# Performance work log

Hardware: AMD Instinct MI355X
Metric: run time of the kernel (lower is better)

Reference implementation:

```python
import jax, jax.numpy as jnp
import numpy as np

D_MODEL = 768
NUM_HEADS = 12
DEPTH = D_MODEL // NUM_HEADS


def setup_inputs() -> dict:
    key = jax.random.key(0)
    ks = jax.random.split(key, 11)
    B, S, D = 2, 2048, D_MODEL
    scale = 1.0 / np.sqrt(D)
    inp = {
        "v": jax.random.normal(ks[0], (B, S, D), jnp.float32),
        "k": jax.random.normal(ks[1], (B, S, D), jnp.float32),
        "q": jax.random.normal(ks[2], (B, S, D), jnp.float32),
        "wq": jax.random.normal(ks[3], (D, D), jnp.float32) * scale,
        "bq": jnp.zeros((D,), jnp.float32),
        "wk": jax.random.normal(ks[4], (D, D), jnp.float32) * scale,
        "bk": jnp.zeros((D,), jnp.float32),
        "wv": jax.random.normal(ks[5], (D, D), jnp.float32) * scale,
        "bv": jnp.zeros((D,), jnp.float32),
        "wo": jax.random.normal(ks[6], (D, D), jnp.float32) * scale,
        "bo": jnp.zeros((D,), jnp.float32),
    }
    return inp


def _split_heads(x):
    # (B, S, D) -> (B, H, S, depth)
    B, S, _ = x.shape
    return x.reshape(B, S, NUM_HEADS, DEPTH).transpose(0, 2, 1, 3)


def reference(v, k, q, wq, bq, wk, bk, wv, bv, wo, bo):
    B, S, D = q.shape
    qh = _split_heads(q @ wq + bq)  # (B,H,S,dh)
    kh = _split_heads(k @ wk + bk)
    vh = _split_heads(v @ wv + bv)
    logits = jnp.einsum("bhqd,bhkd->bhqk", qh, kh) / jnp.sqrt(
        jnp.asarray(DEPTH, qh.dtype)
    )
    attn = jax.nn.softmax(logits, axis=-1)  # (B,H,S,S)
    ctx = jnp.einsum("bhqk,bhkd->bhqd", attn, vh)
    ctx = ctx.transpose(0, 2, 1, 3).reshape(B, S, D)
    return ctx @ wo + bo
```

## Files before the change

kernel.cpp:

```cpp
#include <hip/hip_runtime.h>
#include <hip/hip_bf16.h>
#include <math.h>

typedef __bf16 bf16;
typedef __attribute__((ext_vector_type(8))) __bf16 bf16x8;
typedef __attribute__((ext_vector_type(4))) __bf16 bf16x4v;
typedef __attribute__((ext_vector_type(4))) float f32x4;

#define MFMA16(a, b, c) __builtin_amdgcn_mfma_f32_16x16x32_bf16(a, b, c, 0, 0, 0)

__device__ __forceinline__ void gld16(const bf16* g, bf16* l) {
  __builtin_amdgcn_global_load_lds((const __attribute__((address_space(1))) void*)g,
                                   (__attribute__((address_space(3))) void*)l, 16, 0, 0);
}

__global__ __launch_bounds__(256) void prep(const float* __restrict__ q,
                                            const float* __restrict__ k,
                                            const float* __restrict__ v,
                                            bf16* __restrict__ qb, bf16* __restrict__ kb,
                                            bf16* __restrict__ vb,
                                            const float* __restrict__ w0,
                                            const float* __restrict__ w1,
                                            const float* __restrict__ w2,
                                            const float* __restrict__ w3,
                                            bf16* __restrict__ t0, bf16* __restrict__ t1,
                                            bf16* __restrict__ t2, bf16* __restrict__ t3) {
  const int lin = blockIdx.x;
  if (lin < 4608) {
    const int which = lin / 1536, idx = lin % 1536;
    const float* a = which == 0 ? q : (which == 1 ? k : v);
    bf16* o = which == 0 ? qb : (which == 1 ? kb : vb);
    const size_t i = ((size_t)idx * 256 + threadIdx.x) * 8;
    const float4 f0 = *(const float4*)(a + i);
    const float4 f1 = *(const float4*)(a + i + 4);
    bf16x8 r = {(bf16)f0.x, (bf16)f0.y, (bf16)f0.z, (bf16)f0.w,
                (bf16)f1.x, (bf16)f1.y, (bf16)f1.z, (bf16)f1.w};
    *(bf16x8*)(o + i) = r;
  } else {
    const int w = lin - 4608;
    const int z = w / 576, rem = w % 576;
    const int by = rem / 24, bx = rem % 24;
    const float* W = z == 0 ? w0 : (z == 1 ? w1 : (z == 2 ? w2 : w3));
    bf16* T = z == 0 ? t0 : (z == 1 ? t1 : (z == 2 ? t2 : t3));
    __shared__ float t[32][33];
    const int tx = threadIdx.x & 31, ty = threadIdx.x >> 5;
    const int c0 = bx * 32, r0 = by * 32;
#pragma unroll
    for (int i = 0; i < 4; ++i) {
      const int r = ty + 8 * i;
      t[r][tx] = W[(size_t)(r0 + r) * 768 + c0 + tx];
    }
    __syncthreads();
#pragma unroll
    for (int i = 0; i < 4; ++i) {
      const int r = ty + 8 * i;
      T[(size_t)(c0 + r) * 768 + r0 + tx] = (bf16)t[tx][r];
    }
  }
}

__device__ __forceinline__ void gemm_core(const bf16* __restrict__ A, const bf16* __restrict__ BT,
                                          int row0, int col0, bf16* As, bf16* Bs,
                                          f32x4 acc[4][4]) {
  const int tid = threadIdx.x;
  const int lane = tid & 63, wave = tid >> 6;
  const int m15 = lane & 15, kg = lane >> 4;
  const int wm = wave >> 1, wn = wave & 1;
  const int pr16 = lane & 15;
  const int pk8 = (lane >> 4) * 8;
#pragma unroll
  for (int i = 0; i < 4; ++i)
#pragma unroll
    for (int j = 0; j < 4; ++j) acc[i][j] = f32x4{0.f, 0.f, 0.f, 0.f};

  for (int k0 = 0; k0 < 768; k0 += 32) {
#pragma unroll
    for (int j = 0; j < 2; ++j) {
      const int i = wave * 2 + j;
      gld16(A + (size_t)(row0 + 16 * i + pr16) * 768 + k0 + pk8, As + i * 512);
      gld16(BT + (size_t)(col0 + 16 * i + pr16) * 768 + k0 + pk8, Bs + i * 512);
    }
    __syncthreads();
    bf16x8 af[4], bfr[4];
#pragma unroll
    for (int t = 0; t < 4; ++t)
      af[t] = *(const bf16x8*)(As + (4 * wm + t) * 512 + kg * 128 + m15 * 8);
#pragma unroll
    for (int t = 0; t < 4; ++t)
      bfr[t] = *(const bf16x8*)(Bs + (4 * wn + t) * 512 + kg * 128 + m15 * 8);
#pragma unroll
    for (int mt = 0; mt < 4; ++mt)
#pragma unroll
      for (int nt = 0; nt < 4; ++nt) acc[mt][nt] = MFMA16(af[mt], bfr[nt], acc[mt][nt]);
    __syncthreads();
  }
}

__global__ __launch_bounds__(256, 3) void gemm_qkv(
    const bf16* __restrict__ qb, const bf16* __restrict__ kb, const bf16* __restrict__ vb,
    const bf16* __restrict__ wqT, const bf16* __restrict__ wkT, const bf16* __restrict__ wvT,
    const float* __restrict__ bq, const float* __restrict__ bk, const float* __restrict__ bv,
    bf16* __restrict__ Qh, bf16* __restrict__ Kh, bf16* __restrict__ Vt) {
  __shared__ bf16 As[128 * 32], Bs[128 * 32];
  const bf16 *A, *BT;
  const float* bias;
  bf16* out;
  int mode;
  if (blockIdx.z == 0) { A = qb; BT = wqT; bias = bq; out = Qh; mode = 0; }
  else if (blockIdx.z == 1) { A = kb; BT = wkT; bias = bk; out = Kh; mode = 0; }
  else { A = vb; BT = wvT; bias = bv; out = Vt; mode = 1; }
  const int row0 = blockIdx.y * 128, col0 = blockIdx.x * 128;
  f32x4 acc[4][4];
  gemm_core(A, BT, row0, col0, As, Bs, acc);

  const int lane = threadIdx.x & 63, wave = threadIdx.x >> 6;
  const int m15 = lane & 15, kg = lane >> 4;
  const int wm = wave >> 1, wn = wave & 1;
#pragma unroll
  for (int mt = 0; mt < 4; ++mt) {
#pragma unroll
    for (int nt = 0; nt < 4; ++nt) {
      const int col = col0 + 64 * wn + 16 * nt + m15;
      const float bb = bias[col];
      const int h = col >> 6, d = col & 63;
      const int rowb = row0 + 64 * wm + 16 * mt + kg * 4;
      const int b = rowb >> 11, s0 = rowb & 2047;
      if (mode == 0) {
#pragma unroll
        for (int r = 0; r < 4; ++r)
          out[((size_t)(b * 12 + h) * 2048 + s0 + r) * 64 + d] = (bf16)(acc[mt][nt][r] + bb);
      } else {
        bf16x4v pk;
#pragma unroll
        for (int r = 0; r < 4; ++r) pk[r] = (bf16)(acc[mt][nt][r] + bb);
        *(bf16x4v*)&out[((size_t)(b * 12 + h) * 64 + d) * 2048 + s0] = pk;
      }
    }
  }
}

__global__ __launch_bounds__(256, 3) void gemm_out(const bf16* __restrict__ A,
                                                   const bf16* __restrict__ BT,
                                                   const float* __restrict__ bias,
                                                   float* __restrict__ out) {
  __shared__ bf16 As[64 * 32], Bs[64 * 32];
  const int tid = threadIdx.x;
  const int lane = tid & 63, wave = tid >> 6;
  const int m15 = lane & 15, kg = lane >> 4;
  const int wm = wave >> 1, wn = wave & 1;
  const int row0 = blockIdx.y * 64, col0 = blockIdx.x * 64;
  const int pr16 = lane & 15, pk8 = (lane >> 4) * 8;

  f32x4 acc[2][2];
#pragma unroll
  for (int i = 0; i < 2; ++i)
#pragma unroll
    for (int j = 0; j < 2; ++j) acc[i][j] = f32x4{0.f, 0.f, 0.f, 0.f};

  for (int k0 = 0; k0 < 768; k0 += 32) {
    gld16(A + (size_t)(row0 + 16 * wave + pr16) * 768 + k0 + pk8, As + wave * 512);
    gld16(BT + (size_t)(col0 + 16 * wave + pr16) * 768 + k0 + pk8, Bs + wave * 512);
    __syncthreads();
    bf16x8 af[2], bfr[2];
#pragma unroll
    for (int t = 0; t < 2; ++t)
      af[t] = *(const bf16x8*)(As + (2 * wm + t) * 512 + kg * 128 + m15 * 8);
#pragma unroll
    for (int t = 0; t < 2; ++t)
      bfr[t] = *(const bf16x8*)(Bs + (2 * wn + t) * 512 + kg * 128 + m15 * 8);
#pragma unroll
    for (int mt = 0; mt < 2; ++mt)
#pragma unroll
      for (int nt = 0; nt < 2; ++nt) acc[mt][nt] = MFMA16(af[mt], bfr[nt], acc[mt][nt]);
    __syncthreads();
  }
#pragma unroll
  for (int mt = 0; mt < 2; ++mt) {
#pragma unroll
    for (int nt = 0; nt < 2; ++nt) {
      const int col = col0 + 32 * wn + 16 * nt + m15;
      const float bb = bias[col];
#pragma unroll
      for (int r = 0; r < 4; ++r) {
        const int row = row0 + 32 * wm + 16 * mt + kg * 4 + r;
        out[(size_t)row * 768 + col] = acc[mt][nt][r] + bb;
      }
    }
  }
}

__global__ __launch_bounds__(256, 3) void attn_kernel(const bf16* __restrict__ Q,
                                                      const bf16* __restrict__ K,
                                                      const bf16* __restrict__ VT,
                                                      bf16* __restrict__ ctx) {
  __shared__ __align__(16) bf16 S[21504];

  const int tid = threadIdx.x;
  const int lane = tid & 63, wave = tid >> 6;
  const int m15 = lane & 15, kg = lane >> 4;
  const int lin = blockIdx.x;
  const int bh = lin % 24, qblk = lin / 24;
  const size_t hb = (size_t)bh * 2048 * 64;
  const bf16* Qp = Q + hb;
  const bf16* Kp = K + hb;
  const bf16* Vp = VT + hb;
  const int pipe = wave >> 1;
  const int qrow0 = qblk * 64 + (wave & 1) * 32;
  bf16* Pw = S + 16384 + wave * 1280;

  const int kpr = lane & 7, kpc = (lane >> 3) * 8;
  const int vpr = lane & 15, vpc = (lane >> 4) * 8;

  bf16x8 qf[2][2];
#pragma unroll
  for (int t = 0; t < 2; ++t)
#pragma unroll
    for (int ks = 0; ks < 2; ++ks) {
      bf16x8 tv = *(const bf16x8*)&Qp[(size_t)(qrow0 + 16 * t + m15) * 64 + 32 * ks + kg * 8];
#pragma unroll
      for (int j = 0; j < 8; ++j) tv[j] = (bf16)((float)tv[j] * 0.125f);
      qf[t][ks] = tv;
    }

  f32x4 o[2][4];
  float lp[2][4];
#pragma unroll
  for (int t = 0; t < 2; ++t) {
#pragma unroll
    for (int nt = 0; nt < 4; ++nt) o[t][nt] = f32x4{0.f, 0.f, 0.f, 0.f};
#pragma unroll
    for (int r = 0; r < 4; ++r) lp[t][r] = 0.f;
  }

#pragma unroll
  for (int j = 0; j < 4; ++j) {
    const int idx = wave * 4 + j;
    const int sp = idx >> 3, r8 = idx & 7;
    const int kc = sp * 1024;
    if (r8 < 4)
      gld16(Kp + (size_t)(kc + 8 * r8 + kpr) * 64 + kpc, S + sp * 2 * 2048 + r8 * 512);
    else {
      const int i = r8 - 4;
      gld16(Vp + (size_t)(16 * i + vpr) * 2048 + kc + vpc, S + 8192 + sp * 2 * 2048 + i * 512);
    }
  }

  for (int c = 0; c < 32; ++c) {
    const int buf = c & 1;
    __syncthreads();
    if (c < 31) {
      const int nb = buf ^ 1;
#pragma unroll
      for (int j = 0; j < 4; ++j) {
        const int idx = wave * 4 + j;
        const int sp = idx >> 3, r8 = idx & 7;
        const int kc = sp * 1024 + (c + 1) * 32;
        if (r8 < 4)
          gld16(Kp + (size_t)(kc + 8 * r8 + kpr) * 64 + kpc,
                S + (sp * 2 + nb) * 2048 + r8 * 512);
        else {
          const int i = r8 - 4;
          gld16(Vp + (size_t)(16 * i + vpr) * 2048 + kc + vpc,
                S + 8192 + (sp * 2 + nb) * 2048 + i * 512);
        }
      }
    }
    const bf16* KsB = S + (pipe * 2 + buf) * 2048;
    const bf16* VsB = S + 8192 + (pipe * 2 + buf) * 2048;

    f32x4 s[2][2];
#pragma unroll
    for (int t = 0; t < 2; ++t)
#pragma unroll
      for (int nt = 0; nt < 2; ++nt) s[t][nt] = f32x4{0.f, 0.f, 0.f, 0.f};
#pragma unroll
    for (int ks = 0; ks < 2; ++ks) {
#pragma unroll
      for (int nt = 0; nt < 2; ++nt) {
        const int key = 16 * nt + m15;
        const bf16x8 kf =
            *(const bf16x8*)&KsB[(key >> 3) * 512 + (4 * ks + kg) * 64 + (key & 7) * 8];
        s[0][nt] = MFMA16(qf[0][ks], kf, s[0][nt]);
        s[1][nt] = MFMA16(qf[1][ks], kf, s[1][nt]);
      }
    }
#pragma unroll
    for (int t = 0; t < 2; ++t)
#pragma unroll
      for (int r = 0; r < 4; ++r)
#pragma unroll
        for (int nt = 0; nt < 2; ++nt) {
          const float pe = __expf(s[t][nt][r]);
          lp[t][r] += pe;
          Pw[t * 640 + (kg * 4 + r) * 40 + 16 * nt + m15] = (bf16)pe;
        }
    asm volatile("s_waitcnt lgkmcnt(0)" ::: "memory");
    const bf16x8 pf0 = *(const bf16x8*)&Pw[0 * 640 + m15 * 40 + kg * 8];
    const bf16x8 pf1 = *(const bf16x8*)&Pw[1 * 640 + m15 * 40 + kg * 8];
#pragma unroll
    for (int nt = 0; nt < 4; ++nt) {
      const int d = 16 * nt + m15;
      const bf16x8 vf =
          *(const bf16x8*)&VsB[(d >> 4) * 512 + kg * 128 + (d & 15) * 8];
      o[0][nt] = MFMA16(pf0, vf, o[0][nt]);
      o[1][nt] = MFMA16(pf1, vf, o[1][nt]);
    }
  }

  __syncthreads();
  float* sc = (float*)S;
  if (wave >= 2) {
    const int rg = (wave - 2) * 2560;
#pragma unroll
    for (int t = 0; t < 2; ++t)
#pragma unroll
      for (int nt = 0; nt < 4; ++nt)
        *(f32x4*)&sc[rg + (t * 4 + nt) * 256 + lane * 4] = o[t][nt];
    f32x4 l0 = {lp[0][0], lp[0][1], lp[0][2], lp[0][3]};
    f32x4 l1 = {lp[1][0], lp[1][1], lp[1][2], lp[1][3]};
    *(f32x4*)&sc[rg + 2048 + lane * 8] = l0;
    *(f32x4*)&sc[rg + 2048 + lane * 8 + 4] = l1;
  }
  __syncthreads();
  if (wave < 2) {
    const int rg = wave * 2560;
#pragma unroll
    for (int t = 0; t < 2; ++t)
#pragma unroll
      for (int nt = 0; nt < 4; ++nt) {
        const f32x4 po = *(const f32x4*)&sc[rg + (t * 4 + nt) * 256 + lane * 4];
#pragma unroll
        for (int j = 0; j < 4; ++j) o[t][nt][j] += po[j];
      }
    const f32x4 pl0 = *(const f32x4*)&sc[rg + 2048 + lane * 8];
    const f32x4 pl1 = *(const f32x4*)&sc[rg + 2048 + lane * 8 + 4];
#pragma unroll
    for (int r = 0; r < 4; ++r) { lp[0][r] += pl0[r]; lp[1][r] += pl1[r]; }
#pragma unroll
    for (int t = 0; t < 2; ++t)
#pragma unroll
      for (int r = 0; r < 4; ++r) {
#pragma unroll
        for (int st = 1; st < 16; st <<= 1) lp[t][r] += __shfl_xor(lp[t][r], st);
      }
    const int b = bh / 12, h = bh % 12;
#pragma unroll
    for (int t = 0; t < 2; ++t)
#pragma unroll
      for (int nt = 0; nt < 4; ++nt)
#pragma unroll
        for (int r = 0; r < 4; ++r) {
          const int sr = qrow0 + 16 * t + kg * 4 + r;
          ctx[((size_t)(b * 2048) + sr) * 768 + h * 64 + 16 * nt + m15] =
              (bf16)(o[t][nt][r] / lp[t][r]);
        }
  }
}

extern "C" void kernel_launch(void* const* d_in, const int* in_sizes, int n_in,
                              void* d_out, int out_size, void* d_ws, size_t ws_size,
                              hipStream_t stream) {
  const float* v = (const float*)d_in[0];
  const float* k = (const float*)d_in[1];
  const float* q = (const float*)d_in[2];
  const float* wq = (const float*)d_in[3];
  const float* bq = (const float*)d_in[4];
  const float* wk = (const float*)d_in[5];
  const float* bk = (const float*)d_in[6];
  const float* wv = (const float*)d_in[7];
  const float* bv = (const float*)d_in[8];
  const float* wo = (const float*)d_in[9];
  const float* bo = (const float*)d_in[10];

  char* ws = (char*)d_ws;
  const size_t SEG = (size_t)4096 * 768 * sizeof(bf16);
  const size_t WSEG = (size_t)768 * 768 * sizeof(bf16);
  bf16* Qh = (bf16*)(ws + 0 * SEG);
  bf16* Kh = (bf16*)(ws + 1 * SEG);
  bf16* Vt = (bf16*)(ws + 2 * SEG);
  bf16* qb = (bf16*)(ws + 3 * SEG);
  bf16* kb = (bf16*)(ws + 4 * SEG);
  bf16* vb = (bf16*)(ws + 5 * SEG);
  bf16* ctx = qb;
  bf16* wqT = (bf16*)(ws + 6 * SEG);
  bf16* wkT = (bf16*)(ws + 6 * SEG + WSEG);
  bf16* wvT = (bf16*)(ws + 6 * SEG + 2 * WSEG);
  bf16* woT = (bf16*)(ws + 6 * SEG + 3 * WSEG);

  prep<<<dim3(6912), 256, 0, stream>>>(q, k, v, qb, kb, vb, wq, wk, wv, wo,
                                       wqT, wkT, wvT, woT);
  gemm_qkv<<<dim3(6, 32, 3), 256, 0, stream>>>(qb, kb, vb, wqT, wkT, wvT, bq, bk, bv,
                                               Qh, Kh, Vt);
  attn_kernel<<<dim3(768), 256, 0, stream>>>(Qh, Kh, Vt, ctx);
  gemm_out<<<dim3(12, 64), 256, 0, stream>>>(ctx, woT, bo, (float*)d_out);
}
```

Baseline: 214.2 us.

## Load GEMM fragments directly from global, retile to 96 columns, use exp2 in attention

The QKV and output projection GEMMs drop LDS staging and barriers and read MFMA fragments straight from global memory, with 96-wide column tiles and new grid sizes. The attention kernel folds log2(e) into the Q scaling and uses exp2 instead of exp. Its accumulator arrays are also flattened into separate per-tile variables. The aim is to remove LDS round trips and sync overhead and to cheapen the exponentials, at the cost of redundant global/L2 traffic from losing cross-wave reuse.

```diff
diff --git a/kernel.cpp b/kernel.cpp
--- a/kernel.cpp
+++ b/kernel.cpp
@@ -59,73 +59,62 @@
   }
 }
 
-__device__ __forceinline__ void gemm_core(const bf16* __restrict__ A, const bf16* __restrict__ BT,
-                                          int row0, int col0, bf16* As, bf16* Bs,
-                                          f32x4 acc[4][4]) {
-  const int tid = threadIdx.x;
-  const int lane = tid & 63, wave = tid >> 6;
-  const int m15 = lane & 15, kg = lane >> 4;
-  const int wm = wave >> 1, wn = wave & 1;
-  const int pr16 = lane & 15;
-  const int pk8 = (lane >> 4) * 8;
-#pragma unroll
-  for (int i = 0; i < 4; ++i)
-#pragma unroll
-    for (int j = 0; j < 4; ++j) acc[i][j] = f32x4{0.f, 0.f, 0.f, 0.f};
-
-  for (int k0 = 0; k0 < 768; k0 += 32) {
-#pragma unroll
-    for (int j = 0; j < 2; ++j) {
-      const int i = wave * 2 + j;
-      gld16(A + (size_t)(row0 + 16 * i + pr16) * 768 + k0 + pk8, As + i * 512);
-      gld16(BT + (size_t)(col0 + 16 * i + pr16) * 768 + k0 + pk8, Bs + i * 512);
-    }
-    __syncthreads();
-    bf16x8 af[4], bfr[4];
-#pragma unroll
-    for (int t = 0; t < 4; ++t)
-      af[t] = *(const bf16x8*)(As + (4 * wm + t) * 512 + kg * 128 + m15 * 8);
-#pragma unroll
-    for (int t = 0; t < 4; ++t)
-      bfr[t] = *(const bf16x8*)(Bs + (4 * wn + t) * 512 + kg * 128 + m15 * 8);
-#pragma unroll
-    for (int mt = 0; mt < 4; ++mt)
-#pragma unroll
-      for (int nt = 0; nt < 4; ++nt) acc[mt][nt] = MFMA16(af[mt], bfr[nt], acc[mt][nt]);
-    __syncthreads();
-  }
-}
-
 __global__ __launch_bounds__(256, 3) void gemm_qkv(
     const bf16* __restrict__ qb, const bf16* __restrict__ kb, const bf16* __restrict__ vb,
     const bf16* __restrict__ wqT, const bf16* __restrict__ wkT, const bf16* __restrict__ wvT,
     const float* __restrict__ bq, const float* __restrict__ bk, const float* __restrict__ bv,
     bf16* __restrict__ Qh, bf16* __restrict__ Kh, bf16* __restrict__ Vt) {
-  __shared__ bf16 As[128 * 32], Bs[128 * 32];
   const bf16 *A, *BT;
   const float* bias;
-  bf16* out;
   int mode;
-  if (blockIdx.z == 0) { A = qb; BT = wqT; bias = bq; out = Qh; mode = 0; }
-  else if (blockIdx.z == 1) { A = kb; BT = wkT; bias = bk; out = Kh; mode = 0; }
-  else { A = vb; BT = wvT; bias = bv; out = Vt; mode = 1; }
-  const int row0 = blockIdx.y * 128, col0 = blockIdx.x * 128;
-  f32x4 acc[4][4];
-  gemm_core(A, BT, row0, col0, As, Bs, acc);
-
-  const int lane = threadIdx.x & 63, wave = threadIdx.x >> 6;
+  if (blockIdx.z == 0) { A = qb; BT = wqT; bias = bq; mode = 0; }
+  else if (blockIdx.z == 1) { A = kb; BT = wkT; bias = bk; mode = 0; }
+  else { A = vb; BT = wvT; bias = bv; mode = 1; }
+  const int row0 = blockIdx.y * 128, col0 = blockIdx.x * 96;
+
+  const int tid = threadIdx.x;
+  const int lane = tid & 63, wave = tid >> 6;
   const int m15 = lane & 15, kg = lane >> 4;
   const int wm = wave >> 1, wn = wave & 1;
+
+  const bf16* Ab[4];
+  const bf16* Bb[3];
+#pragma unroll
+  for (int t = 0; t < 4; ++t)
+    Ab[t] = A + (size_t)(row0 + 64 * wm + 16 * t + m15) * 768 + kg * 8;
+#pragma unroll
+  for (int t = 0; t < 3; ++t)
+    Bb[t] = BT + (size_t)(col0 + 48 * wn + 16 * t + m15) * 768 + kg * 8;
+
+  f32x4 acc[4][3];
+#pragma unroll
+  for (int i = 0; i < 4; ++i)
+#pragma unroll
+    for (int j = 0; j < 3; ++j) acc[i][j] = f32x4{0.f, 0.f, 0.f, 0.f};
+
+  for (int k0 = 0; k0 < 768; k0 += 32) {
+    bf16x8 af[4], bfr[3];
+#pragma unroll
+    for (int t = 0; t < 4; ++t) af[t] = *(const bf16x8*)(Ab[t] + k0);
+#pragma unroll
+    for (int t = 0; t < 3; ++t) bfr[t] = *(const bf16x8*)(Bb[t] + k0);
+#pragma unroll
+    for (int mt = 0; mt < 4; ++mt)
+#pragma unroll
+      for (int nt = 0; nt < 3; ++nt) acc[mt][nt] = MFMA16(af[mt], bfr[nt], acc[mt][nt]);
+  }
+
 #pragma unroll
   for (int mt = 0; mt < 4; ++mt) {
 #pragma unroll
-    for (int nt = 0; nt < 4; ++nt) {
-      const int col = col0 + 64 * wn + 16 * nt + m15;
+    for (int nt = 0; nt < 3; ++nt) {
+      const int col = col0 + 48 * wn + 16 * nt + m15;
       const float bb = bias[col];
       const int h = col >> 6, d = col & 63;
       const int rowb = row0 + 64 * wm + 16 * mt + kg * 4;
       const int b = rowb >> 11, s0 = rowb & 2047;
       if (mode == 0) {
+        bf16* out = (blockIdx.z == 0) ? Qh : Kh;
 #pragma unroll
         for (int r = 0; r < 4; ++r)
           out[((size_t)(b * 12 + h) * 2048 + s0 + r) * 64 + d] = (bf16)(acc[mt][nt][r] + bb);
@@ -133,52 +122,53 @@
         bf16x4v pk;
 #pragma unroll
         for (int r = 0; r < 4; ++r) pk[r] = (bf16)(acc[mt][nt][r] + bb);
-        *(bf16x4v*)&out[((size_t)(b * 12 + h) * 64 + d) * 2048 + s0] = pk;
-      }
-    }
-  }
-}
-
-__global__ __launch_bounds__(256, 3) void gemm_out(const bf16* __restrict__ A,
+        *(bf16x4v*)&Vt[((size_t)(b * 12 + h) * 64 + d) * 2048 + s0] = pk;
+      }
+    }
+  }
+}
+
+__global__ __launch_bounds__(256, 4) void gemm_out(const bf16* __restrict__ A,
                                                    const bf16* __restrict__ BT,
                                                    const float* __restrict__ bias,
                                                    float* __restrict__ out) {
-  __shared__ bf16 As[64 * 32], Bs[64 * 32];
   const int tid = threadIdx.x;
   const int lane = tid & 63, wave = tid >> 6;
   const int m15 = lane & 15, kg = lane >> 4;
   const int wm = wave >> 1, wn = wave & 1;
-  const int row0 = blockIdx.y * 64, col0 = blockIdx.x * 64;
-  const int pr16 = lane & 15, pk8 = (lane >> 4) * 8;
-
-  f32x4 acc[2][2];
+  const int row0 = blockIdx.y * 64, col0 = blockIdx.x * 96;
+
+  const bf16* Ab[2];
+  const bf16* Bb[3];
+#pragma unroll
+  for (int t = 0; t < 2; ++t)
+    Ab[t] = A + (size_t)(row0 + 32 * wm + 16 * t + m15) * 768 + kg * 8;
+#pragma unroll
+  for (int t = 0; t < 3; ++t)
+    Bb[t] = BT + (size_t)(col0 + 48 * wn + 16 * t + m15) * 768 + kg * 8;
+
+  f32x4 acc[2][3];
 #pragma unroll
   for (int i = 0; i < 2; ++i)
 #pragma unroll
-    for (int j = 0; j < 2; ++j) acc[i][j] = f32x4{0.f, 0.f, 0.f, 0.f};
+    for (int j = 0; j < 3; ++j) acc[i][j] = f32x4{0.f, 0.f, 0.f, 0.f};
 
   for (int k0 = 0; k0 < 768; k0 += 32) {
-    gld16(A + (size_t)(row0 + 16 * wave + pr16) * 768 + k0 + pk8, As + wave * 512);
-    gld16(BT + (size_t)(col0 + 16 * wave + pr16) * 768 + k0 + pk8, Bs + wave * 512);
-    __syncthreads();
-    bf16x8 af[2], bfr[2];
-#pragma unroll
-    for (int t = 0; t < 2; ++t)
-      af[t] = *(const bf16x8*)(As + (2 * wm + t) * 512 + kg * 128 + m15 * 8);
-#pragma unroll
-    for (int t = 0; t < 2; ++t)
-      bfr[t] = *(const bf16x8*)(Bs + (2 * wn + t) * 512 + kg * 128 + m15 * 8);
+    bf16x8 af[2], bfr[3];
+#pragma unroll
+    for (int t = 0; t < 2; ++t) af[t] = *(const bf16x8*)(Ab[t] + k0);
+#pragma unroll
+    for (int t = 0; t < 3; ++t) bfr[t] = *(const bf16x8*)(Bb[t] + k0);
 #pragma unroll
     for (int mt = 0; mt < 2; ++mt)
 #pragma unroll
-      for (int nt = 0; nt < 2; ++nt) acc[mt][nt] = MFMA16(af[mt], bfr[nt], acc[mt][nt]);
-    __syncthreads();
+      for (int nt = 0; nt < 3; ++nt) acc[mt][nt] = MFMA16(af[mt], bfr[nt], acc[mt][nt]);
   }
 #pragma unroll
   for (int mt = 0; mt < 2; ++mt) {
 #pragma unroll
-    for (int nt = 0; nt < 2; ++nt) {
-      const int col = col0 + 32 * wn + 16 * nt + m15;
+    for (int nt = 0; nt < 3; ++nt) {
+      const int col = col0 + 48 * wn + 16 * nt + m15;
       const float bb = bias[col];
 #pragma unroll
       for (int r = 0; r < 4; ++r) {
@@ -218,19 +208,16 @@
     for (int ks = 0; ks < 2; ++ks) {
       bf16x8 tv = *(const bf16x8*)&Qp[(size_t)(qrow0 + 16 * t + m15) * 64 + 32 * ks + kg * 8];
 #pragma unroll
-      for (int j = 0; j < 8; ++j) tv[j] = (bf16)((float)tv[j] * 0.125f);
+      for (int j = 0; j < 8; ++j) tv[j] = (bf16)((float)tv[j] * 0.18033688011f);
       qf[t][ks] = tv;
     }
 
-  f32x4 o[2][4];
-  float lp[2][4];
-#pragma unroll
-  for (int t = 0; t < 2; ++t) {
-#pragma unroll
-    for (int nt = 0; nt < 4; ++nt) o[t][nt] = f32x4{0.f, 0.f, 0.f, 0.f};
-#pragma unroll
-    for (int r = 0; r < 4; ++r) lp[t][r] = 0.f;
-  }
+  f32x4 o0[4], o1[4];
+  float lp0[4], lp1[4];
+#pragma unroll
+  for (int nt = 0; nt < 4; ++nt) { o0[nt] = f32x4{0.f, 0.f, 0.f, 0.f}; o1[nt] = f32x4{0.f, 0.f, 0.f, 0.f}; }
+#pragma unroll
+  for (int r = 0; r < 4; ++r) { lp0[r] = 0.f; lp1[r] = 0.f; }
 
 #pragma unroll
   for (int j = 0; j < 4; ++j) {
@@ -268,11 +255,9 @@
     const bf16* KsB = S + (pipe * 2 + buf) * 2048;
     const bf16* VsB = S + 8192 + (pipe * 2 + buf) * 2048;
 
-    f32x4 s[2][2];
-#pragma unroll
-    for (int t = 0; t < 2; ++t)
-#pragma unroll
-      for (int nt = 0; nt < 2; ++nt) s[t][nt] = f32x4{0.f, 0.f, 0.f, 0.f};
+    f32x4 s0[2], s1[2];
+#pragma unroll
+    for (int nt = 0; nt < 2; ++nt) { s0[nt] = f32x4{0.f, 0.f, 0.f, 0.f}; s1[nt] = f32x4{0.f, 0.f, 0.f, 0.f}; }
 #pragma unroll
     for (int ks = 0; ks < 2; ++ks) {
 #pragma unroll
@@ -280,20 +265,21 @@
         const int key = 16 * nt + m15;
         const bf16x8 kf =
             *(const bf16x8*)&KsB[(key >> 3) * 512 + (4 * ks + kg) * 64 + (key & 7) * 8];
-        s[0][nt] = MFMA16(qf[0][ks], kf, s[0][nt]);
-        s[1][nt] = MFMA16(qf[1][ks], kf, s[1][nt]);
-      }
-    }
-#pragma unroll
-    for (int t = 0; t < 2; ++t)
-#pragma unroll
-      for (int r = 0; r < 4; ++r)
-#pragma unroll
-        for (int nt = 0; nt < 2; ++nt) {
-          const float pe = __expf(s[t][nt][r]);
-          lp[t][r] += pe;
-          Pw[t * 640 + (kg * 4 + r) * 40 + 16 * nt + m15] = (bf16)pe;
-        }
+        s0[nt] = MFMA16(qf[0][ks], kf, s0[nt]);
+        s1[nt] = MFMA16(qf[1][ks], kf, s1[nt]);
+      }
+    }
+#pragma unroll
+    for (int r = 0; r < 4; ++r)
+#pragma unroll
+      for (int nt = 0; nt < 2; ++nt) {
+        const float p0 = __builtin_exp2f(s0[nt][r]);
+        const float p1 = __builtin_exp2f(s1[nt][r]);
+        lp0[r] += p0;
+        lp1[r] += p1;
+        Pw[0 * 640 + (kg * 4 + r) * 40 + 16 * nt + m15] = (bf16)p0;
+        Pw[1 * 640 + (kg * 4 + r) * 40 + 16 * nt + m15] = (bf16)p1;
+      }
     asm volatile("s_waitcnt lgkmcnt(0)" ::: "memory");
     const bf16x8 pf0 = *(const bf16x8*)&Pw[0 * 640 + m15 * 40 + kg * 8];
     const bf16x8 pf1 = *(const bf16x8*)&Pw[1 * 640 + m15 * 40 + kg * 8];
@@ -302,8 +288,8 @@
       const int d = 16 * nt + m15;
       const bf16x8 vf =
           *(const bf16x8*)&VsB[(d >> 4) * 512 + kg * 128 + (d & 15) * 8];
-      o[0][nt] = MFMA16(pf0, vf, o[0][nt]);
-      o[1][nt] = MFMA16(pf1, vf, o[1][nt]);
+      o0[nt] = MFMA16(pf0, vf, o0[nt]);
+      o1[nt] = MFMA16(pf1, vf, o1[nt]);
     }
   }
 
@@ -315,9 +301,9 @@
     for (int t = 0; t < 2; ++t)
 #pragma unroll
       for (int nt = 0; nt < 4; ++nt)
-        *(f32x4*)&sc[rg + (t * 4 + nt) * 256 + lane * 4] = o[t][nt];
-    f32x4 l0 = {lp[0][0], lp[0][1], lp[0][2], lp[0][3]};
-    f32x4 l1 = {lp[1][0], lp[1][1], lp[1][2], lp[1][3]};
+        *(f32x4*)&sc[rg + (t * 4 + nt) * 256 + lane * 4] = (t == 0) ? o0[nt] : o1[nt];
+    f32x4 l0 = {lp0[0], lp0[1], lp0[2], lp0[3]};
+    f32x4 l1 = {lp1[0], lp1[1], lp1[2], lp1[3]};
     *(f32x4*)&sc[rg + 2048 + lane * 8] = l0;
     *(f32x4*)&sc[rg + 2048 + lane * 8 + 4] = l1;
   }
@@ -325,35 +311,33 @@
   if (wave < 2) {
     const int rg = wave * 2560;
 #pragma unroll
-    for (int t = 0; t < 2; ++t)
-#pragma unroll
-      for (int nt = 0; nt < 4; ++nt) {
-        const f32x4 po = *(const f32x4*)&sc[rg + (t * 4 + nt) * 256 + lane * 4];
-#pragma unroll
-        for (int j = 0; j < 4; ++j) o[t][nt][j] += po[j];
-      }
+    for (int nt = 0; nt < 4; ++nt) {
+      const f32x4 p0 = *(const f32x4*)&sc[rg + (0 * 4 + nt) * 256 + lane * 4];
+      const f32x4 p1 = *(const f32x4*)&sc[rg + (1 * 4 + nt) * 256 + lane * 4];
+#pragma unroll
+      for (int j = 0; j < 4; ++j) { o0[nt][j] += p0[j]; o1[nt][j] += p1[j]; }
+    }
     const f32x4 pl0 = *(const f32x4*)&sc[rg + 2048 + lane * 8];
     const f32x4 pl1 = *(const f32x4*)&sc[rg + 2048 + lane * 8 + 4];
 #pragma unroll
-    for (int r = 0; r < 4; ++r) { lp[0][r] += pl0[r]; lp[1][r] += pl1[r]; }
-#pragma unroll
-    for (int t = 0; t < 2; ++t)
+    for (int r = 0; r < 4; ++r) { lp0[r] += pl0[r]; lp1[r] += pl1[r]; }
+#pragma unroll
+    for (int r = 0; r < 4; ++r) {
+#pragma unroll
+      for (int st = 1; st < 16; st <<= 1) {
+        lp0[r] += __shfl_xor(lp0[r], st);
+        lp1[r] += __shfl_xor(lp1[r], st);
+      }
+    }
+    const int b = bh / 12, h = bh % 12;
+#pragma unroll
+    for (int nt = 0; nt < 4; ++nt)
 #pragma unroll
       for (int r = 0; r < 4; ++r) {
-#pragma unroll
-        for (int st = 1; st < 16; st <<= 1) lp[t][r] += __shfl_xor(lp[t][r], st);
-      }
-    const int b = bh / 12, h = bh % 12;
-#pragma unroll
-    for (int t = 0; t < 2; ++t)
-#pragma unroll
-      for (int nt = 0; nt < 4; ++nt)
-#pragma unroll
-        for (int r = 0; r < 4; ++r) {
-          const int sr = qrow0 + 16 * t + kg * 4 + r;
-          ctx[((size_t)(b * 2048) + sr) * 768 + h * 64 + 16 * nt + m15] =
-              (bf16)(o[t][nt][r] / lp[t][r]);
-        }
+        const int sr0 = qrow0 + kg * 4 + r;
+        ctx[((size_t)(b * 2048) + sr0) * 768 + h * 64 + 16 * nt + m15] = (bf16)(o0[nt][r] / lp0[r]);
+        ctx[((size_t)(b * 2048) + sr0 + 16) * 768 + h * 64 + 16 * nt + m15] = (bf16)(o1[nt][r] / lp1[r]);
+      }
   }
 }
 
@@ -389,8 +373,8 @@
 
   prep<<<dim3(6912), 256, 0, stream>>>(q, k, v, qb, kb, vb, wq, wk, wv, wo,
                                        wqT, wkT, wvT, woT);
-  gemm_qkv<<<dim3(6, 32, 3), 256, 0, stream>>>(qb, kb, vb, wqT, wkT, wvT, bq, bk, bv,
+  gemm_qkv<<<dim3(8, 32, 3), 256, 0, stream>>>(qb, kb, vb, wqT, wkT, wvT, bq, bk, bv,
                                                Qh, Kh, Vt);
   attn_kernel<<<dim3(768), 256, 0, stream>>>(Qh, Kh, Vt, ctx);
-  gemm_out<<<dim3(12, 64), 256, 0, stream>>>(ctx, woT, bo, (float*)d_out);
-}
+  gemm_out<<<dim3(8, 64), 256, 0, stream>>>(ctx, woT, bo, (float*)d_out);
+}
```

New measurement: 247.2 us. 15.4% more time.
